# Kernel tuning notes

Hardware: AMD Instinct MI355X
Metric: run time of the kernel (lower is better)

Reference implementation:

```python
import jax, jax.numpy as jnp
import numpy as np

EMB = 1024
HEADS = 16
HEAD_DIM = EMB // HEADS
FF = 4 * EMB
EPS = 1e-5


def setup_inputs() -> dict:
    key = jax.random.key(0)
    ks = jax.random.split(key, 16)
    s = 0.02
    return {
        "x": jax.random.normal(ks[0], (2, 2048, EMB), dtype=jnp.float32),
        "ln1_g": jnp.ones((EMB,), jnp.float32),
        "ln1_b": jnp.zeros((EMB,), jnp.float32),
        "Wq": jax.random.normal(ks[1], (EMB, EMB), jnp.float32) * s,
        "bq": jnp.zeros((EMB,), jnp.float32),
        "Wk": jax.random.normal(ks[2], (EMB, EMB), jnp.float32) * s,
        "bk": jnp.zeros((EMB,), jnp.float32),
        "Wv": jax.random.normal(ks[3], (EMB, EMB), jnp.float32) * s,
        "bv": jnp.zeros((EMB,), jnp.float32),
        "Wo": jax.random.normal(ks[4], (EMB, EMB), jnp.float32) * s,
        "bo": jnp.zeros((EMB,), jnp.float32),
        "ln2_g": jnp.ones((EMB,), jnp.float32),
        "ln2_b": jnp.zeros((EMB,), jnp.float32),
        "W1": jax.random.normal(ks[5], (EMB, FF), jnp.float32) * s,
        "b1": jnp.zeros((FF,), jnp.float32),
        "W2": jax.random.normal(ks[6], (FF, EMB), jnp.float32) * s,
        "b2": jnp.zeros((EMB,), jnp.float32),
    }


def _layernorm(x, g, b):
    mu = jnp.mean(x, axis=-1, keepdims=True)
    var = jnp.var(x, axis=-1, keepdims=True)
    return (x - mu) * jax.lax.rsqrt(var + EPS) * g + b


def _attention(x, Wq, bq, Wk, bk, Wv, bv, Wo, bo):
    B, T, C = x.shape
    # [B,T,C] -> [B,H,T,Dh]
    def split(y):
        return y.reshape(B, T, HEADS, HEAD_DIM).transpose(0, 2, 1, 3)
    Q = split(x @ Wq + bq)
    K = split(x @ Wk + bk)
    V = split(x @ Wv + bv)
    att = jnp.einsum("bhqd,bhkd->bhqk", Q, K) / np.sqrt(HEAD_DIM).astype(np.float32)
    causal = jnp.tril(jnp.ones((T, T), bool))
    att = jnp.where(causal, att, -jnp.inf)
    att = jax.nn.softmax(att, axis=-1)
    out = jnp.einsum("bhqk,bhkd->bhqd", att, V)
    out = out.transpose(0, 2, 1, 3).reshape(B, T, C)
    return out @ Wo + bo


def reference(x, ln1_g, ln1_b, Wq, bq, Wk, bk, Wv, bv, Wo, bo,
              ln2_g, ln2_b, W1, b1, W2, b2):
    # dropout is identity in eval mode
    x = x + _attention(_layernorm(x, ln1_g, ln1_b), Wq, bq, Wk, bk, Wv, bv, Wo, bo)
    h = _layernorm(x, ln2_g, ln2_b)
    h = jax.nn.gelu(h @ W1 + b1, approximate=False) @ W2 + b2
    return x + h
```

## Files before the change

kernel.cpp:

```cpp
#include <hip/hip_runtime.h>
#include <hip/hip_bf16.h>

typedef __attribute__((ext_vector_type(4))) float f32x4;
typedef __attribute__((ext_vector_type(8))) short bf16x8;
typedef unsigned int u32;
typedef unsigned short u16;

#define GASP __attribute__((address_space(1)))
#define LASP __attribute__((address_space(3)))

__device__ __forceinline__ u16 f2bf(float f) {
  u32 u = __float_as_uint(f);
  return (u16)((u + 0x7fffu + ((u >> 16) & 1u)) >> 16);
}

__device__ __forceinline__ u32 cvtpk(float lo, float hi) {
  u32 r;
  asm("v_cvt_pk_bf16_f32 %0, %1, %2" : "=v"(r) : "v"(lo), "v"(hi));
  return r;
}

__device__ __forceinline__ void gl_lds16(const void* g, void* l) {
  __builtin_amdgcn_global_load_lds((const GASP u32*)g, (LASP u32*)l, 16, 0, 0);
}

struct CastArgs {
  const float* s[6];
  u16* d[6];
};

__global__ __launch_bounds__(256) void cast_w(CastArgs a) {
  int bid = blockIdx.x;
  int w, t, K, N, kshift;
  if (bid < 4096)      { w = bid >> 10; t = bid & 1023; K = 1024; N = 1024; kshift = 5; }
  else if (bid < 8192) { w = 4; t = bid - 4096; K = 1024; N = 4096; kshift = 5; }
  else                 { w = 5; t = bid - 8192; K = 4096; N = 1024; kshift = 7; }
  int tk = t & ((1 << kshift) - 1);
  int tn = t >> kshift;
  int k0 = tk << 5, n0 = tn << 5;
  const float* src = a.s[w];
  u16* dst = a.d[w];
  __shared__ u16 tile[32][36];
  int r = threadIdx.x >> 3, c0 = (threadIdx.x & 7) << 2;
  float4 v = *(const float4*)&src[(size_t)(k0 + r) * N + n0 + c0];
  tile[c0 + 0][r] = f2bf(v.x);
  tile[c0 + 1][r] = f2bf(v.y);
  tile[c0 + 2][r] = f2bf(v.z);
  tile[c0 + 3][r] = f2bf(v.w);
  __syncthreads();
  ushort4 o;
  o.x = tile[r][c0 + 0];
  o.y = tile[r][c0 + 1];
  o.z = tile[r][c0 + 2];
  o.w = tile[r][c0 + 3];
  *(ushort4*)&dst[(size_t)(n0 + r) * K + k0 + c0] = o;
}

__global__ __launch_bounds__(256) void ln_k(const float* __restrict__ x, const float* __restrict__ g,
                                            const float* __restrict__ b, u16* __restrict__ out) {
  int row = blockIdx.x;
  int tid = threadIdx.x;
  float4 v = *(const float4*)&x[(size_t)row * 1024 + tid * 4];
  float s = v.x + v.y + v.z + v.w;
  float ss = v.x * v.x + v.y * v.y + v.z * v.z + v.w * v.w;
#pragma unroll
  for (int o = 32; o >= 1; o >>= 1) {
    s += __shfl_xor(s, o, 64);
    ss += __shfl_xor(ss, o, 64);
  }
  __shared__ float red[8];
  int wv = tid >> 6;
  if ((tid & 63) == 0) { red[wv] = s; red[wv + 4] = ss; }
  __syncthreads();
  s = red[0] + red[1] + red[2] + red[3];
  ss = red[4] + red[5] + red[6] + red[7];
  float mu = s * (1.0f / 1024.0f);
  float var = ss * (1.0f / 1024.0f) - mu * mu;
  float rstd = rsqrtf(var + 1e-5f);
  float4 gv = *(const float4*)&g[tid * 4];
  float4 bv = *(const float4*)&b[tid * 4];
  ushort4 o4;
  o4.x = f2bf((v.x - mu) * rstd * gv.x + bv.x);
  o4.y = f2bf((v.y - mu) * rstd * gv.y + bv.y);
  o4.z = f2bf((v.z - mu) * rstd * gv.z + bv.z);
  o4.w = f2bf((v.w - mu) * rstd * gv.w + bv.w);
  *(ushort4*)&out[(size_t)row * 1024 + tid * 4] = o4;
}

template <int MODE>
__global__ __launch_bounds__(512, 2) void gemm_256(
    const u16* __restrict__ A, const u16* __restrict__ Bt,
    const float* __restrict__ bias0, const float* __restrict__ bias1, const float* __restrict__ bias2,
    void* outp, int rm, int rn, int xn, int M, int N, int K) {
  __shared__ __align__(16) u16 As[4][128 * 64];
  __shared__ __align__(16) u16 Bs[4][128 * 64];
  char* asB = (char*)As;
  char* bsB = (char*)Bs;
  const int tid = threadIdx.x;
  const int w = tid >> 6, lane = tid & 63;
  const int xcd = blockIdx.x & 7, idx = blockIdx.x >> 3;
  const int mt = (xcd / xn) * rm + (idx % rm);
  const int nt = (xcd % xn) * rn + (idx / rm);
  const int m0 = mt << 8, n0 = nt << 8;

  const int rA = tid >> 3;
  const int csw = ((tid & 7) ^ (rA & 7)) * 8;
  const u16* pA = A + (size_t)(m0 + rA) * K + csw;
  const u16* pB = Bt + (size_t)(n0 + rA) * K + csw;
  const int dstOff = tid * 16;

#define STG_A(kt, h, d_) do {                                            \
    const u16* s_ = pA + (size_t)((h) * 128) * K + (size_t)(kt) * 64;    \
    char* l_ = asB + ((d_) * 2 + (h)) * 16384 + dstOff;                  \
    gl_lds16(s_, l_);                                                    \
    gl_lds16(s_ + (size_t)64 * K, l_ + 8192);                            \
  } while (0)
#define STG_B(kt, h, d_) do {                                            \
    const u16* s_ = pB + (size_t)((h) * 128) * K + (size_t)(kt) * 64;    \
    char* l_ = bsB + ((d_) * 2 + (h)) * 16384 + dstOff;                  \
    gl_lds16(s_, l_);                                                    \
    gl_lds16(s_ + (size_t)64 * K, l_ + 8192);                            \
  } while (0)

  const int wr = w >> 2, wc = w & 3;
  const int g = lane >> 4, qi = lane & 15;

  int aOff[8][2], bOff[4][2];
#pragma unroll
  for (int mm = 0; mm < 8; ++mm) {
    int row = mm * 16 + qi;
#pragma unroll
    for (int ks = 0; ks < 2; ++ks)
      aOff[mm][ks] = row * 128 + (((ks * 4 + g) ^ (qi & 7)) << 4);
  }
#pragma unroll
  for (int nn = 0; nn < 4; ++nn) {
    int rowb = (wc & 1) * 64 + nn * 16 + qi;
#pragma unroll
    for (int ks = 0; ks < 2; ++ks)
      bOff[nn][ks] = rowb * 128 + (((ks * 4 + g) ^ (qi & 7)) << 4);
  }

  f32x4 acc[8][4];
#pragma unroll
  for (int i = 0; i < 8; ++i)
#pragma unroll
    for (int j = 0; j < 4; ++j) acc[i][j] = f32x4{0.f, 0.f, 0.f, 0.f};

#define MFMA16(MB, A00, A01, A10, A11) do {                                              \
    __builtin_amdgcn_s_setprio(1);                                                       \
    acc[(MB)][0] = __builtin_amdgcn_mfma_f32_16x16x32_bf16(A00, bv[0][0], acc[(MB)][0], 0, 0, 0); \
    acc[(MB)][1] = __builtin_amdgcn_mfma_f32_16x16x32_bf16(A00, bv[1][0], acc[(MB)][1], 0, 0, 0); \
    acc[(MB)][2] = __builtin_amdgcn_mfma_f32_16x16x32_bf16(A00, bv[2][0], acc[(MB)][2], 0, 0, 0); \
    acc[(MB)][3] = __builtin_amdgcn_mfma_f32_16x16x32_bf16(A00, bv[3][0], acc[(MB)][3], 0, 0, 0); \
    acc[(MB) + 1][0] = __builtin_amdgcn_mfma_f32_16x16x32_bf16(A10, bv[0][0], acc[(MB) + 1][0], 0, 0, 0); \
    acc[(MB) + 1][1] = __builtin_amdgcn_mfma_f32_16x16x32_bf16(A10, bv[1][0], acc[(MB) + 1][1], 0, 0, 0); \
    acc[(MB) + 1][2] = __builtin_amdgcn_mfma_f32_16x16x32_bf16(A10, bv[2][0], acc[(MB) + 1][2], 0, 0, 0); \
    acc[(MB) + 1][3] = __builtin_amdgcn_mfma_f32_16x16x32_bf16(A10, bv[3][0], acc[(MB) + 1][3], 0, 0, 0); \
    acc[(MB)][0] = __builtin_amdgcn_mfma_f32_16x16x32_bf16(A01, bv[0][1], acc[(MB)][0], 0, 0, 0); \
    acc[(MB)][1] = __builtin_amdgcn_mfma_f32_16x16x32_bf16(A01, bv[1][1], acc[(MB)][1], 0, 0, 0); \
    acc[(MB)][2] = __builtin_amdgcn_mfma_f32_16x16x32_bf16(A01, bv[2][1], acc[(MB)][2], 0, 0, 0); \
    acc[(MB)][3] = __builtin_amdgcn_mfma_f32_16x16x32_bf16(A01, bv[3][1], acc[(MB)][3], 0, 0, 0); \
    acc[(MB) + 1][0] = __builtin_amdgcn_mfma_f32_16x16x32_bf16(A11, bv[0][1], acc[(MB) + 1][0], 0, 0, 0); \
    acc[(MB) + 1][1] = __builtin_amdgcn_mfma_f32_16x16x32_bf16(A11, bv[1][1], acc[(MB) + 1][1], 0, 0, 0); \
    acc[(MB) + 1][2] = __builtin_amdgcn_mfma_f32_16x16x32_bf16(A11, bv[2][1], acc[(MB) + 1][2], 0, 0, 0); \
    acc[(MB) + 1][3] = __builtin_amdgcn_mfma_f32_16x16x32_bf16(A11, bv[3][1], acc[(MB) + 1][3], 0, 0, 0); \
    __builtin_amdgcn_s_setprio(0);                                                       \
  } while (0)

#define RDA(dst0, dst1, MB)                                          \
    bf16x8 dst0##0 = *(const bf16x8*)(asB + aTB + aOff[(MB)][0]);     \
    bf16x8 dst0##1 = *(const bf16x8*)(asB + aTB + aOff[(MB)][1]);     \
    bf16x8 dst1##0 = *(const bf16x8*)(asB + aTB + aOff[(MB) + 1][0]); \
    bf16x8 dst1##1 = *(const bf16x8*)(asB + aTB + aOff[(MB) + 1][1]);

  const int T = K >> 6;
  STG_A(0, 0, 0); STG_A(0, 1, 0);
  STG_B(0, 0, 0); STG_B(0, 1, 0);
  asm volatile("s_waitcnt vmcnt(0)" ::: "memory");
  __builtin_amdgcn_s_barrier();

  for (int t = 0; t < T; ++t) {
    const int d = t & 1;
    const int aTB = (d * 2 + wr) * 16384;
    const int bTB = (d * 2 + (wc >> 1)) * 16384;
    bf16x8 bv[4][2];
#pragma unroll
    for (int nn = 0; nn < 4; ++nn) {
      bv[nn][0] = *(const bf16x8*)(bsB + bTB + bOff[nn][0]);
      bv[nn][1] = *(const bf16x8*)(bsB + bTB + bOff[nn][1]);
    }
    RDA(p0a, p0b, 0);
    if (t + 1 < T) STG_A(t + 1, 0, d ^ 1);
    MFMA16(0, p0a0, p0a1, p0b0, p0b1);
    RDA(p1a, p1b, 2);
    if (t + 1 < T) STG_A(t + 1, 1, d ^ 1);
    MFMA16(2, p1a0, p1a1, p1b0, p1b1);
    RDA(p2a, p2b, 4);
    if (t + 1 < T) STG_B(t + 1, 0, d ^ 1);
    MFMA16(4, p2a0, p2a1, p2b0, p2b1);
    RDA(p3a, p3b, 6);
    if (t + 1 < T) STG_B(t + 1, 1, d ^ 1);
    MFMA16(6, p3a0, p3a1, p3b0, p3b1);
    asm volatile("" ::: "memory");
    if (t + 1 < T) { asm volatile("s_waitcnt vmcnt(0)" ::: "memory"); }
    __builtin_amdgcn_s_barrier();
  }
#undef MFMA16
#undef RDA
#undef STG_A
#undef STG_B

  const int ci = lane & 15;
#pragma unroll
  for (int mm = 0; mm < 8; ++mm) {
#pragma unroll
    for (int nn = 0; nn < 4; ++nn) {
      int colb = n0 + wc * 64 + nn * 16 + ci;
      int rowbase = m0 + wr * 128 + mm * 16 + 4 * g;
      f32x4 c = acc[mm][nn];
      if constexpr (MODE == 2) {
        int sel = colb >> 10;
        int cc = colb & 1023;
        const float* bp = sel == 0 ? bias0 : (sel == 1 ? bias1 : bias2);
        float bb = bp[cc];
        int h = cc >> 6, dd = cc & 63;
        int b_ = rowbase >> 11, tt = rowbase & 2047;
        if (sel == 2) {
          u16* op = (u16*)outp + 2ull * (4096ull * 1024ull);
          ushort4 o4;
          o4.x = f2bf(c[0] + bb);
          o4.y = f2bf(c[1] + bb);
          o4.z = f2bf(c[2] + bb);
          o4.w = f2bf(c[3] + bb);
          *(ushort4*)&op[((size_t)(b_ * 16 + h) * 64 + dd) * 2048 + tt] = o4;
        } else {
          float scale = (sel == 0) ? 0.125f : 1.0f;
          u16* op = (u16*)outp + (size_t)sel * (4096ull * 1024ull);
#pragma unroll
          for (int r = 0; r < 4; ++r)
            op[((size_t)(b_ * 16 + h) * 2048 + tt + r) * 64 + dd] = f2bf((c[r] + bb) * scale);
        }
      } else {
        float bb = bias0[colb];
#pragma unroll
        for (int r = 0; r < 4; ++r) {
          float v = c[r] + bb;
          float gl = 0.5f * v * (1.0f + erff(v * 0.70710678118654752f));
          ((u16*)outp)[(size_t)(rowbase + r) * N + colb] = f2bf(gl);
        }
      }
    }
  }
}

__global__ __launch_bounds__(512) void gemm_sk(
    const u16* __restrict__ A, const u16* __restrict__ Bt,
    const float* __restrict__ bias0, float* __restrict__ outp,
    const float* __restrict__ res, int M, int N, int K) {
  __shared__ __align__(16) union SM {
    struct { u16 As[2][4][128 * 32]; u16 Bs[2][4][128 * 32]; } t;
    float red[16][4][4][64];
  } sm;
  const int tid = threadIdx.x;
  const int w8 = tid >> 6, lane = tid & 63;
  const int gg = w8 >> 2, wl = w8 & 3;
  const int m0 = blockIdx.y << 7, n0 = blockIdx.x << 7;

  char* asB = (char*)sm.t.As[gg];
  char* bsB = (char*)sm.t.Bs[gg];
  const u16* aS[2];
  const u16* bS[2];
#pragma unroll
  for (int i = 0; i < 2; ++i) {
    int p = wl * 2048 + i * 1024 + lane * 16;
    int r = p >> 6;
    int cl = ((p >> 4) & 3) ^ ((r >> 1) & 3);
    aS[i] = A + (size_t)(m0 + r) * K + gg * 32 + cl * 8;
    bS[i] = Bt + (size_t)(n0 + r) * K + gg * 32 + cl * 8;
  }
  f32x4 acc[4][4];
#pragma unroll
  for (int i = 0; i < 4; ++i)
#pragma unroll
    for (int j = 0; j < 4; ++j) acc[i][j] = f32x4{0.f, 0.f, 0.f, 0.f};

  const int wr = wl >> 1, wc = wl & 1;
  int aOff[4], bOff[4];
#pragma unroll
  for (int mm = 0; mm < 4; ++mm) {
    int rowa = wr * 64 + mm * 16 + (lane & 15);
    aOff[mm] = rowa * 64 + (((lane >> 4) ^ ((rowa >> 1) & 3)) << 4);
    int rowb = wc * 64 + mm * 16 + (lane & 15);
    bOff[mm] = rowb * 64 + (((lane >> 4) ^ ((rowb >> 1) & 3)) << 4);
  }

  gl_lds16(aS[0], asB + wl * 2048);
  gl_lds16(aS[1], asB + wl * 2048 + 1024);
  gl_lds16(bS[0], bsB + wl * 2048);
  gl_lds16(bS[1], bsB + wl * 2048 + 1024);
  if (K > 64) {
    gl_lds16(aS[0] + 64, asB + 8192 + wl * 2048);
    gl_lds16(aS[1] + 64, asB + 8192 + wl * 2048 + 1024);
    gl_lds16(bS[0] + 64, bsB + 8192 + wl * 2048);
    gl_lds16(bS[1] + 64, bsB + 8192 + wl * 2048 + 1024);
  }
  if (K > 128) {
    gl_lds16(aS[0] + 128, asB + 16384 + wl * 2048);
    gl_lds16(aS[1] + 128, asB + 16384 + wl * 2048 + 1024);
    gl_lds16(bS[0] + 128, bsB + 16384 + wl * 2048);
    gl_lds16(bS[1] + 128, bsB + 16384 + wl * 2048 + 1024);
  }
  int buf = 0;
  for (int ks = 0; ks < K; ks += 64) {
    const int rem = ((K - ks) >> 6) - 1;
    if (rem >= 2)      { asm volatile("s_waitcnt vmcnt(8)" ::: "memory"); }
    else if (rem == 1) { asm volatile("s_waitcnt vmcnt(4)" ::: "memory"); }
    else               { asm volatile("s_waitcnt vmcnt(0)" ::: "memory"); }
    __builtin_amdgcn_s_barrier();
    asm volatile("" ::: "memory");
    if (ks + 192 < K) {
      const int nb = ((buf + 3) & 3) * 8192;
      gl_lds16(aS[0] + ks + 192, asB + nb + wl * 2048);
      gl_lds16(aS[1] + ks + 192, asB + nb + wl * 2048 + 1024);
      gl_lds16(bS[0] + ks + 192, bsB + nb + wl * 2048);
      gl_lds16(bS[1] + ks + 192, bsB + nb + wl * 2048 + 1024);
    }
    const int tb = buf * 8192;
    bf16x8 av[4], bv[4];
#pragma unroll
    for (int mm = 0; mm < 4; ++mm) av[mm] = *(const bf16x8*)(asB + tb + aOff[mm]);
#pragma unroll
    for (int nn = 0; nn < 4; ++nn) bv[nn] = *(const bf16x8*)(bsB + tb + bOff[nn]);
#pragma unroll
    for (int mm = 0; mm < 4; ++mm)
#pragma unroll
      for (int nn = 0; nn < 4; ++nn)
        acc[mm][nn] = __builtin_amdgcn_mfma_f32_16x16x32_bf16(av[mm], bv[nn], acc[mm][nn], 0, 0, 0);
    buf = (buf + 1) & 3;
  }

  __syncthreads();
  if (gg == 1) {
#pragma unroll
    for (int mm = 0; mm < 4; ++mm)
#pragma unroll
      for (int nn = 0; nn < 4; ++nn)
#pragma unroll
        for (int r = 0; r < 4; ++r) sm.red[mm * 4 + nn][r][wl][lane] = acc[mm][nn][r];
  }
  __syncthreads();
  if (gg == 0) {
    const int g = lane >> 4, ci = lane & 15;
#pragma unroll
    for (int mm = 0; mm < 4; ++mm) {
#pragma unroll
      for (int nn = 0; nn < 4; ++nn) {
        int colb = n0 + wc * 64 + nn * 16 + ci;
        int rowbase = m0 + wr * 64 + mm * 16 + 4 * g;
        float bb = bias0[colb];
#pragma unroll
        for (int r = 0; r < 4; ++r) {
          size_t idx = (size_t)(rowbase + r) * N + colb;
          outp[idx] = acc[mm][nn][r] + sm.red[mm * 4 + nn][r][wl][lane] + bb + res[idx];
        }
      }
    }
  }
}

__global__ __launch_bounds__(512) void attn_k(const u16* __restrict__ Q, const u16* __restrict__ Kg,
                                              const u16* __restrict__ Vt, u16* __restrict__ O) {
  __shared__ __align__(16) u16 Ks[2][64 * 64];
  __shared__ __align__(16) u16 Vs[2][64 * 64];
  const int bx = blockIdx.y;
  const int bh = blockIdx.x;
  const int tid = threadIdx.x, w = tid >> 6, lane = tid & 63;
  const int g = lane >> 4, qi = lane & 15;
  const u16* Qb = Q + (size_t)bh * 2048 * 64;
  const u16* Kb = Kg + (size_t)bh * 2048 * 64;
  const u16* Vtb = Vt + (size_t)bh * 64 * 2048;

  const int rS = tid >> 3, cS = tid & 7;
  const int csw = (cS ^ (rS & 7)) * 8;
  const u16* srcK = Kb + (size_t)rS * 64 + csw;
  const u16* srcV = Vtb + (size_t)rS * 2048 + csw;
  char* ksB = (char*)Ks;
  char* vsB = (char*)Vs;
  const int dstOff = tid * 16;

  int koff[4][2], voff[4][2];
#pragma unroll
  for (int t = 0; t < 4; ++t) {
    int row = 16 * t + qi;
#pragma unroll
    for (int h = 0; h < 2; ++h) koff[t][h] = row * 128 + (((4 * h + g) ^ (qi & 7)) << 4);
#pragma unroll
    for (int kt = 0; kt < 2; ++kt) voff[t][kt] = row * 128 + (((4 * kt + g) ^ (qi & 7)) << 4);
  }

  const int b_ = bh >> 4, hh = bh & 15;
  u32* Ou = (u32*)O;

  for (int job = 0; job < 2; ++job) {
    const int qt = job ? bx : 15 - bx;
    const int qmin = qt * 128 + w * 16;
    const int qrow = qmin + qi;
    const int qmaxw = qmin + 15;

    bf16x8 qf[2];
#pragma unroll
    for (int h = 0; h < 2; ++h)
      qf[h] = *(const bf16x8*)(Qb + (size_t)qrow * 64 + h * 32 + g * 8);

    f32x4 acc[4];
#pragma unroll
    for (int dt = 0; dt < 4; ++dt) acc[dt] = f32x4{0.f, 0.f, 0.f, 0.f};
    float m = -1e30f, lsum = 0.0f;

    __syncthreads();
    gl_lds16(srcK, ksB + dstOff);
    gl_lds16(srcV, vsB + dstOff);

    const int nsteps = 2 * qt + 2;
    int buf = 0;
    for (int s = 0; s < nsteps; ++s) {
      __syncthreads();
      if (s + 1 < nsteps) {
        int nb = buf ^ 1;
        gl_lds16(srcK + (size_t)(s + 1) * 4096, ksB + nb * 8192 + dstOff);
        gl_lds16(srcV + (size_t)(s + 1) * 64, vsB + nb * 8192 + dstOff);
      }
      const int kv0 = s * 64;
      if (kv0 <= qmaxw) {
        const int tb = buf * 8192;
        f32x4 st[4];
        __builtin_amdgcn_s_setprio(1);
#pragma unroll
        for (int t = 0; t < 4; ++t) {
          st[t] = f32x4{0.f, 0.f, 0.f, 0.f};
#pragma unroll
          for (int h = 0; h < 2; ++h) {
            bf16x8 kf = *(const bf16x8*)(ksB + tb + koff[t][h]);
            st[t] = __builtin_amdgcn_mfma_f32_16x16x32_bf16(kf, qf[h], st[t], 0, 0, 0);
          }
        }
        __builtin_amdgcn_s_setprio(0);
        float pvv[4][4];
        float tmax = -1e30f;
        if (kv0 + 63 > qmin) {
#pragma unroll
          for (int t = 0; t < 4; ++t)
#pragma unroll
            for (int r = 0; r < 4; ++r) {
              int key = kv0 + 16 * t + 4 * g + r;
              float sv = st[t][r];
              sv = (key <= qrow) ? sv : -1e30f;
              pvv[t][r] = sv;
              tmax = fmaxf(tmax, sv);
            }
        } else {
#pragma unroll
          for (int t = 0; t < 4; ++t)
#pragma unroll
            for (int r = 0; r < 4; ++r) {
              float sv = st[t][r];
              pvv[t][r] = sv;
              tmax = fmaxf(tmax, sv);
            }
        }
        tmax = fmaxf(tmax, __shfl_xor(tmax, 16, 64));
        tmax = fmaxf(tmax, __shfl_xor(tmax, 32, 64));
        if (!__all(tmax <= m + 8.0f)) {
          float mn = fmaxf(m, tmax);
          float corr = __expf(m - mn);
          lsum *= corr;
#pragma unroll
          for (int dt = 0; dt < 4; ++dt)
#pragma unroll
            for (int r = 0; r < 4; ++r) acc[dt][r] *= corr;
          m = mn;
        }
        float tsum = 0.f;
#pragma unroll
        for (int t = 0; t < 4; ++t)
#pragma unroll
          for (int r = 0; r < 4; ++r) {
            float e = __expf(pvv[t][r] - m);
            pvv[t][r] = e;
            tsum += e;
          }
        tsum += __shfl_xor(tsum, 16, 64);
        tsum += __shfl_xor(tsum, 32, 64);
        lsum += tsum;
        u32 pk[4][2], ex[4][2];
#pragma unroll
        for (int t = 0; t < 4; ++t)
#pragma unroll
          for (int p = 0; p < 2; ++p) {
            u32 v = cvtpk(pvv[t][2 * p], pvv[t][2 * p + 1]);
            pk[t][p] = v;
            ex[t][p] = (u32)__shfl_xor((int)v, 16, 64);
          }
        const bool ge = (g & 1) == 0;
        const bool G0 = (g >> 1) == 0;
        const bool innr = (g == 0) || (g == 3);
        u32 mm_[4][4];
#pragma unroll
        for (int t = 0; t < 4; ++t) {
          mm_[t][0] = ge ? pk[t][0] : ex[t][0];
          mm_[t][1] = ge ? pk[t][1] : ex[t][1];
          mm_[t][2] = ge ? ex[t][0] : pk[t][0];
          mm_[t][3] = ge ? ex[t][1] : pk[t][1];
        }
        union Frag { u32 u[4]; bf16x8 v; } f0, f1;
#pragma unroll
        for (int i = 0; i < 4; ++i) {
          u32 sel0 = G0 ? mm_[1][i] : mm_[0][i];
          u32 sel1 = G0 ? mm_[3][i] : mm_[2][i];
          u32 sw0 = (u32)__shfl_xor((int)sel0, 32, 64);
          u32 sw1 = (u32)__shfl_xor((int)sel1, 32, 64);
          u32 own0 = G0 ? mm_[0][i] : mm_[1][i];
          u32 own1 = G0 ? mm_[2][i] : mm_[3][i];
          f0.u[i] = innr ? own0 : sw0;
          f1.u[i] = innr ? own1 : sw1;
        }
        __builtin_amdgcn_s_setprio(1);
#pragma unroll
        for (int dt = 0; dt < 4; ++dt) {
          bf16x8 vfa = *(const bf16x8*)(vsB + tb + voff[dt][0]);
          acc[dt] = __builtin_amdgcn_mfma_f32_16x16x32_bf16(vfa, f0.v, acc[dt], 0, 0, 0);
          bf16x8 vfb = *(const bf16x8*)(vsB + tb + voff[dt][1]);
          acc[dt] = __builtin_amdgcn_mfma_f32_16x16x32_bf16(vfb, f1.v, acc[dt], 0, 0, 0);
        }
        __builtin_amdgcn_s_setprio(0);
      }
      buf ^= 1;
    }

    float rl = 1.0f / lsum;
    size_t rowq = (size_t)(b_ * 2048 + qrow);
#pragma unroll
    for (int dt = 0; dt < 4; ++dt) {
#pragma unroll
      for (int rp = 0; rp < 2; ++rp) {
        u16 lo = f2bf(acc[dt][rp * 2] * rl);
        u16 hi = f2bf(acc[dt][rp * 2 + 1] * rl);
        u32 pkd = (u32)lo | ((u32)hi << 16);
        size_t off = rowq * 1024 + hh * 64 + dt * 16 + 4 * g + rp * 2;
        Ou[off >> 1] = pkd;
      }
    }
  }
}

extern "C" void kernel_launch(void* const* d_in, const int* in_sizes, int n_in,
                              void* d_out, int out_size, void* d_ws, size_t ws_size,
                              hipStream_t stream) {
  const float* x    = (const float*)d_in[0];
  const float* ln1g = (const float*)d_in[1];
  const float* ln1b = (const float*)d_in[2];
  const float* Wq   = (const float*)d_in[3];
  const float* bq   = (const float*)d_in[4];
  const float* Wk   = (const float*)d_in[5];
  const float* bk   = (const float*)d_in[6];
  const float* Wv   = (const float*)d_in[7];
  const float* bv   = (const float*)d_in[8];
  const float* Wo   = (const float*)d_in[9];
  const float* bo   = (const float*)d_in[10];
  const float* ln2g = (const float*)d_in[11];
  const float* ln2b = (const float*)d_in[12];
  const float* W1   = (const float*)d_in[13];
  const float* b1   = (const float*)d_in[14];
  const float* W2   = (const float*)d_in[15];
  const float* b2   = (const float*)d_in[16];

  char* ws = (char*)d_ws;
  const size_t MB = 1ull << 20;
  u16* WqT = (u16*)(ws + 0 * MB);
  u16* WkT = (u16*)(ws + 2 * MB);
  u16* WvT = (u16*)(ws + 4 * MB);
  u16* WoT = (u16*)(ws + 6 * MB);
  u16* W1T = (u16*)(ws + 8 * MB);
  u16* W2T = (u16*)(ws + 16 * MB);
  u16* XN  = (u16*)(ws + 24 * MB);
  u16* Qb  = (u16*)(ws + 32 * MB);
  u16* Kb  = (u16*)(ws + 40 * MB);
  u16* Vtb = (u16*)(ws + 48 * MB);
  u16* Ob  = (u16*)(ws + 56 * MB);
  u16* Gb  = (u16*)(ws + 32 * MB);

  CastArgs ca;
  ca.s[0] = Wq; ca.s[1] = Wk; ca.s[2] = Wv; ca.s[3] = Wo; ca.s[4] = W1; ca.s[5] = W2;
  ca.d[0] = WqT; ca.d[1] = WkT; ca.d[2] = WvT; ca.d[3] = WoT; ca.d[4] = W1T; ca.d[5] = W2T;
  cast_w<<<12288, 256, 0, stream>>>(ca);

  ln_k<<<4096, 256, 0, stream>>>(x, ln1g, ln1b, XN);

  gemm_256<2><<<192, 512, 0, stream>>>(XN, WqT, bq, bk, bv, Qb, 4, 6, 2, 4096, 3072, 1024);

  attn_k<<<dim3(32, 8), 512, 0, stream>>>(Qb, Kb, Vtb, Ob);

  gemm_sk<<<dim3(8, 32), 512, 0, stream>>>(Ob, WoT, bo, (float*)d_out, x, 4096, 1024, 1024);

  ln_k<<<4096, 256, 0, stream>>>((const float*)d_out, ln2g, ln2b, XN);

  gemm_256<3><<<256, 512, 0, stream>>>(XN, W1T, b1, nullptr, nullptr, Gb, 8, 4, 4, 4096, 4096, 1024);

  gemm_sk<<<dim3(8, 32), 512, 0, stream>>>(Gb, W2T, b2, (float*)d_out, (const float*)d_out, 4096, 1024, 4096);
}
```

Measured before the change: 235.3 us.

## Restructure attention to 4 waves with two query tiles per wave sharing K/V fragments

The attention kernel now runs 256-thread blocks, where each wave owns 32 query rows (two 16-row tiles) instead of 16. K and V fragments loaded from LDS are reused across both tiles. The old two-job paired scheduling is replaced by one q-tile per block, with a 32x16 grid and launch_bounds(256,2). This halves LDS fragment reads per query and improves MFMA density, at the cost of more registers and losing the explicit causal load balancing between short and long q-tiles.

```diff
diff --git a/kernel.cpp b/kernel.cpp
--- a/kernel.cpp
+++ b/kernel.cpp
@@ -369,11 +369,11 @@
   }
 }
 
-__global__ __launch_bounds__(512) void attn_k(const u16* __restrict__ Q, const u16* __restrict__ Kg,
-                                              const u16* __restrict__ Vt, u16* __restrict__ O) {
+__global__ __launch_bounds__(256, 2) void attn_k(const u16* __restrict__ Q, const u16* __restrict__ Kg,
+                                                 const u16* __restrict__ Vt, u16* __restrict__ O) {
   __shared__ __align__(16) u16 Ks[2][64 * 64];
   __shared__ __align__(16) u16 Vs[2][64 * 64];
-  const int bx = blockIdx.y;
+  const int qt = 15 - (int)blockIdx.y;
   const int bh = blockIdx.x;
   const int tid = threadIdx.x, w = tid >> 6, lane = tid & 63;
   const int g = lane >> 4, qi = lane & 15;
@@ -381,171 +381,222 @@
   const u16* Kb = Kg + (size_t)bh * 2048 * 64;
   const u16* Vtb = Vt + (size_t)bh * 64 * 2048;
 
-  const int rS = tid >> 3, cS = tid & 7;
-  const int csw = (cS ^ (rS & 7)) * 8;
-  const u16* srcK = Kb + (size_t)rS * 64 + csw;
-  const u16* srcV = Vtb + (size_t)rS * 2048 + csw;
+  const int c1 = 256 + tid;
+  const int r0 = tid >> 3, r1 = c1 >> 3;
+  const int s0 = ((tid & 7) ^ (r0 & 7)) * 8, s1 = ((c1 & 7) ^ (r1 & 7)) * 8;
+  const u16* srcK0 = Kb + (size_t)r0 * 64 + s0;
+  const u16* srcK1 = Kb + (size_t)r1 * 64 + s1;
+  const u16* srcV0 = Vtb + (size_t)r0 * 2048 + s0;
+  const u16* srcV1 = Vtb + (size_t)r1 * 2048 + s1;
   char* ksB = (char*)Ks;
   char* vsB = (char*)Vs;
-  const int dstOff = tid * 16;
+  const int d0 = tid * 16, d1 = c1 * 16;
 
   int koff[4][2], voff[4][2];
 #pragma unroll
   for (int t = 0; t < 4; ++t) {
     int row = 16 * t + qi;
 #pragma unroll
-    for (int h = 0; h < 2; ++h) koff[t][h] = row * 128 + (((4 * h + g) ^ (qi & 7)) << 4);
-#pragma unroll
-    for (int kt = 0; kt < 2; ++kt) voff[t][kt] = row * 128 + (((4 * kt + g) ^ (qi & 7)) << 4);
+    for (int kk = 0; kk < 2; ++kk) {
+      koff[t][kk] = row * 128 + (((4 * kk + g) ^ (qi & 7)) << 4);
+      voff[t][kk] = koff[t][kk];
+    }
   }
 
   const int b_ = bh >> 4, hh = bh & 15;
   u32* Ou = (u32*)O;
 
-  for (int job = 0; job < 2; ++job) {
-    const int qt = job ? bx : 15 - bx;
-    const int qmin = qt * 128 + w * 16;
-    const int qrow = qmin + qi;
-    const int qmaxw = qmin + 15;
-
-    bf16x8 qf[2];
-#pragma unroll
-    for (int h = 0; h < 2; ++h)
-      qf[h] = *(const bf16x8*)(Qb + (size_t)qrow * 64 + h * 32 + g * 8);
-
-    f32x4 acc[4];
-#pragma unroll
-    for (int dt = 0; dt < 4; ++dt) acc[dt] = f32x4{0.f, 0.f, 0.f, 0.f};
-    float m = -1e30f, lsum = 0.0f;
-
+  const int qmin = qt * 128 + w * 32;
+  const int qr0 = qmin + qi, qr1 = qmin + 16 + qi;
+
+  bf16x8 qf[2][2];
+#pragma unroll
+  for (int h = 0; h < 2; ++h)
+#pragma unroll
+    for (int kk = 0; kk < 2; ++kk)
+      qf[h][kk] = *(const bf16x8*)(Qb + (size_t)(qmin + 16 * h + qi) * 64 + kk * 32 + g * 8);
+
+  f32x4 acc0[4], acc1[4];
+#pragma unroll
+  for (int dt = 0; dt < 4; ++dt) {
+    acc0[dt] = f32x4{0.f, 0.f, 0.f, 0.f};
+    acc1[dt] = f32x4{0.f, 0.f, 0.f, 0.f};
+  }
+  float m0 = -1e30f, l0 = 0.0f, m1 = -1e30f, l1 = 0.0f;
+
+  const bool ge = (g & 1) == 0;
+  const bool G0 = (g >> 1) == 0;
+  const bool innr = (g == 0) || (g == 3);
+  union Frag { u32 u[4]; bf16x8 v; };
+
+#define SOFTPACK(ST, ACC, MVAR, LVAR, QROW, F0, F1) do {                      \
+    float pvv[4][4];                                                          \
+    float tmax = -1e30f;                                                      \
+    if (kv0 + 63 > qmin) {                                                    \
+      _Pragma("unroll")                                                       \
+      for (int t = 0; t < 4; ++t)                                             \
+        _Pragma("unroll")                                                     \
+        for (int r = 0; r < 4; ++r) {                                         \
+          int key = kv0 + 16 * t + 4 * g + r;                                 \
+          float sv = ST[t][r];                                                \
+          sv = (key <= (QROW)) ? sv : -1e30f;                                 \
+          pvv[t][r] = sv;                                                     \
+          tmax = fmaxf(tmax, sv);                                             \
+        }                                                                     \
+    } else {                                                                  \
+      _Pragma("unroll")                                                       \
+      for (int t = 0; t < 4; ++t)                                             \
+        _Pragma("unroll")                                                     \
+        for (int r = 0; r < 4; ++r) {                                         \
+          float sv = ST[t][r];                                                \
+          pvv[t][r] = sv;                                                     \
+          tmax = fmaxf(tmax, sv);                                             \
+        }                                                                     \
+    }                                                                         \
+    tmax = fmaxf(tmax, __shfl_xor(tmax, 16, 64));                             \
+    tmax = fmaxf(tmax, __shfl_xor(tmax, 32, 64));                             \
+    if (!__all(tmax <= MVAR + 8.0f)) {                                        \
+      float mn = fmaxf(MVAR, tmax);                                           \
+      float corr = __expf(MVAR - mn);                                         \
+      LVAR *= corr;                                                           \
+      _Pragma("unroll")                                                       \
+      for (int dt = 0; dt < 4; ++dt)                                          \
+        _Pragma("unroll")                                                     \
+        for (int r = 0; r < 4; ++r) ACC[dt][r] *= corr;                       \
+      MVAR = mn;                                                              \
+    }                                                                         \
+    float tsum = 0.f;                                                         \
+    _Pragma("unroll")                                                         \
+    for (int t = 0; t < 4; ++t)                                               \
+      _Pragma("unroll")                                                       \
+      for (int r = 0; r < 4; ++r) {                                           \
+        float e = __expf(pvv[t][r] - MVAR);                                   \
+        pvv[t][r] = e;                                                        \
+        tsum += e;                                                            \
+      }                                                                       \
+    tsum += __shfl_xor(tsum, 16, 64);                                         \
+    tsum += __shfl_xor(tsum, 32, 64);                                         \
+    LVAR += tsum;                                                             \
+    u32 pk[4][2], ex[4][2];                                                   \
+    _Pragma("unroll")                                                         \
+    for (int t = 0; t < 4; ++t)                                               \
+      _Pragma("unroll")                                                       \
+      for (int p = 0; p < 2; ++p) {                                           \
+        u32 v = cvtpk(pvv[t][2 * p], pvv[t][2 * p + 1]);                      \
+        pk[t][p] = v;                                                         \
+        ex[t][p] = (u32)__shfl_xor((int)v, 16, 64);                           \
+      }                                                                       \
+    u32 mm_[4][4];                                                            \
+    _Pragma("unroll")                                                         \
+    for (int t = 0; t < 4; ++t) {                                             \
+      mm_[t][0] = ge ? pk[t][0] : ex[t][0];                                   \
+      mm_[t][1] = ge ? pk[t][1] : ex[t][1];                                   \
+      mm_[t][2] = ge ? ex[t][0] : pk[t][0];                                   \
+      mm_[t][3] = ge ? ex[t][1] : pk[t][1];                                   \
+    }                                                                         \
+    _Pragma("unroll")                                                         \
+    for (int i = 0; i < 4; ++i) {                                             \
+      u32 sel0 = G0 ? mm_[1][i] : mm_[0][i];                                  \
+      u32 sel1 = G0 ? mm_[3][i] : mm_[2][i];                                  \
+      u32 sw0 = (u32)__shfl_xor((int)sel0, 32, 64);                           \
+      u32 sw1 = (u32)__shfl_xor((int)sel1, 32, 64);                           \
+      u32 own0 = G0 ? mm_[0][i] : mm_[1][i];                                  \
+      u32 own1 = G0 ? mm_[2][i] : mm_[3][i];                                  \
+      F0.u[i] = innr ? own0 : sw0;                                            \
+      F1.u[i] = innr ? own1 : sw1;                                            \
+    }                                                                         \
+  } while (0)
+
+  gl_lds16(srcK0, ksB + d0);
+  gl_lds16(srcK1, ksB + d1);
+  gl_lds16(srcV0, vsB + d0);
+  gl_lds16(srcV1, vsB + d1);
+
+  const int nsteps = 2 * qt + 2;
+  int buf = 0;
+  for (int s = 0; s < nsteps; ++s) {
     __syncthreads();
-    gl_lds16(srcK, ksB + dstOff);
-    gl_lds16(srcV, vsB + dstOff);
-
-    const int nsteps = 2 * qt + 2;
-    int buf = 0;
-    for (int s = 0; s < nsteps; ++s) {
-      __syncthreads();
-      if (s + 1 < nsteps) {
-        int nb = buf ^ 1;
-        gl_lds16(srcK + (size_t)(s + 1) * 4096, ksB + nb * 8192 + dstOff);
-        gl_lds16(srcV + (size_t)(s + 1) * 64, vsB + nb * 8192 + dstOff);
-      }
-      const int kv0 = s * 64;
-      if (kv0 <= qmaxw) {
-        const int tb = buf * 8192;
-        f32x4 st[4];
-        __builtin_amdgcn_s_setprio(1);
-#pragma unroll
-        for (int t = 0; t < 4; ++t) {
-          st[t] = f32x4{0.f, 0.f, 0.f, 0.f};
-#pragma unroll
-          for (int h = 0; h < 2; ++h) {
-            bf16x8 kf = *(const bf16x8*)(ksB + tb + koff[t][h]);
-            st[t] = __builtin_amdgcn_mfma_f32_16x16x32_bf16(kf, qf[h], st[t], 0, 0, 0);
-          }
-        }
-        __builtin_amdgcn_s_setprio(0);
-        float pvv[4][4];
-        float tmax = -1e30f;
-        if (kv0 + 63 > qmin) {
-#pragma unroll
-          for (int t = 0; t < 4; ++t)
-#pragma unroll
-            for (int r = 0; r < 4; ++r) {
-              int key = kv0 + 16 * t + 4 * g + r;
-              float sv = st[t][r];
-              sv = (key <= qrow) ? sv : -1e30f;
-              pvv[t][r] = sv;
-              tmax = fmaxf(tmax, sv);
-            }
-        } else {
-#pragma unroll
-          for (int t = 0; t < 4; ++t)
-#pragma unroll
-            for (int r = 0; r < 4; ++r) {
-              float sv = st[t][r];
-              pvv[t][r] = sv;
-              tmax = fmaxf(tmax, sv);
-            }
-        }
-        tmax = fmaxf(tmax, __shfl_xor(tmax, 16, 64));
-        tmax = fmaxf(tmax, __shfl_xor(tmax, 32, 64));
-        if (!__all(tmax <= m + 8.0f)) {
-          float mn = fmaxf(m, tmax);
-          float corr = __expf(m - mn);
-          lsum *= corr;
-#pragma unroll
-          for (int dt = 0; dt < 4; ++dt)
-#pragma unroll
-            for (int r = 0; r < 4; ++r) acc[dt][r] *= corr;
-          m = mn;
-        }
-        float tsum = 0.f;
-#pragma unroll
-        for (int t = 0; t < 4; ++t)
-#pragma unroll
-          for (int r = 0; r < 4; ++r) {
-            float e = __expf(pvv[t][r] - m);
-            pvv[t][r] = e;
-            tsum += e;
-          }
-        tsum += __shfl_xor(tsum, 16, 64);
-        tsum += __shfl_xor(tsum, 32, 64);
-        lsum += tsum;
-        u32 pk[4][2], ex[4][2];
-#pragma unroll
-        for (int t = 0; t < 4; ++t)
-#pragma unroll
-          for (int p = 0; p < 2; ++p) {
-            u32 v = cvtpk(pvv[t][2 * p], pvv[t][2 * p + 1]);
-            pk[t][p] = v;
-            ex[t][p] = (u32)__shfl_xor((int)v, 16, 64);
-          }
-        const bool ge = (g & 1) == 0;
-        const bool G0 = (g >> 1) == 0;
-        const bool innr = (g == 0) || (g == 3);
-        u32 mm_[4][4];
-#pragma unroll
-        for (int t = 0; t < 4; ++t) {
-          mm_[t][0] = ge ? pk[t][0] : ex[t][0];
-          mm_[t][1] = ge ? pk[t][1] : ex[t][1];
-          mm_[t][2] = ge ? ex[t][0] : pk[t][0];
-          mm_[t][3] = ge ? ex[t][1] : pk[t][1];
-        }
-        union Frag { u32 u[4]; bf16x8 v; } f0, f1;
-#pragma unroll
-        for (int i = 0; i < 4; ++i) {
-          u32 sel0 = G0 ? mm_[1][i] : mm_[0][i];
-          u32 sel1 = G0 ? mm_[3][i] : mm_[2][i];
-          u32 sw0 = (u32)__shfl_xor((int)sel0, 32, 64);
-          u32 sw1 = (u32)__shfl_xor((int)sel1, 32, 64);
-          u32 own0 = G0 ? mm_[0][i] : mm_[1][i];
-          u32 own1 = G0 ? mm_[2][i] : mm_[3][i];
-          f0.u[i] = innr ? own0 : sw0;
-          f1.u[i] = innr ? own1 : sw1;
-        }
-        __builtin_amdgcn_s_setprio(1);
-#pragma unroll
-        for (int dt = 0; dt < 4; ++dt) {
-          bf16x8 vfa = *(const bf16x8*)(vsB + tb + voff[dt][0]);
-          acc[dt] = __builtin_amdgcn_mfma_f32_16x16x32_bf16(vfa, f0.v, acc[dt], 0, 0, 0);
-          bf16x8 vfb = *(const bf16x8*)(vsB + tb + voff[dt][1]);
-          acc[dt] = __builtin_amdgcn_mfma_f32_16x16x32_bf16(vfb, f1.v, acc[dt], 0, 0, 0);
-        }
-        __builtin_amdgcn_s_setprio(0);
-      }
-      buf ^= 1;
-    }
-
-    float rl = 1.0f / lsum;
-    size_t rowq = (size_t)(b_ * 2048 + qrow);
+    if (s + 1 < nsteps) {
+      int nb = buf ^ 1;
+      gl_lds16(srcK0 + (size_t)(s + 1) * 4096, ksB + nb * 8192 + d0);
+      gl_lds16(srcK1 + (size_t)(s + 1) * 4096, ksB + nb * 8192 + d1);
+      gl_lds16(srcV0 + (size_t)(s + 1) * 64, vsB + nb * 8192 + d0);
+      gl_lds16(srcV1 + (size_t)(s + 1) * 64, vsB + nb * 8192 + d1);
+    }
+    const int kv0 = s * 64;
+    if (kv0 <= qmin + 31) {
+      const int tb = buf * 8192;
+      bf16x8 kf[4][2];
+#pragma unroll
+      for (int t = 0; t < 4; ++t) {
+        kf[t][0] = *(const bf16x8*)(ksB + tb + koff[t][0]);
+        kf[t][1] = *(const bf16x8*)(ksB + tb + koff[t][1]);
+      }
+      f32x4 st0[4], st1[4];
+      __builtin_amdgcn_s_setprio(1);
+#pragma unroll
+      for (int t = 0; t < 4; ++t) {
+        st0[t] = f32x4{0.f, 0.f, 0.f, 0.f};
+        st0[t] = __builtin_amdgcn_mfma_f32_16x16x32_bf16(kf[t][0], qf[0][0], st0[t], 0, 0, 0);
+        st0[t] = __builtin_amdgcn_mfma_f32_16x16x32_bf16(kf[t][1], qf[0][1], st0[t], 0, 0, 0);
+      }
+#pragma unroll
+      for (int t = 0; t < 4; ++t) {
+        st1[t] = f32x4{0.f, 0.f, 0.f, 0.f};
+        st1[t] = __builtin_amdgcn_mfma_f32_16x16x32_bf16(kf[t][0], qf[1][0], st1[t], 0, 0, 0);
+        st1[t] = __builtin_amdgcn_mfma_f32_16x16x32_bf16(kf[t][1], qf[1][1], st1[t], 0, 0, 0);
+      }
+      __builtin_amdgcn_s_setprio(0);
+      bf16x8 vfa[4], vfb[4];
+#pragma unroll
+      for (int dt = 0; dt < 4; ++dt) {
+        vfa[dt] = *(const bf16x8*)(vsB + tb + voff[dt][0]);
+        vfb[dt] = *(const bf16x8*)(vsB + tb + voff[dt][1]);
+      }
+      Frag f00, f10, f01, f11;
+      SOFTPACK(st0, acc0, m0, l0, qr0, f00, f10);
+      SOFTPACK(st1, acc1, m1, l1, qr1, f01, f11);
+      __builtin_amdgcn_s_setprio(1);
+#pragma unroll
+      for (int dt = 0; dt < 4; ++dt) {
+        acc0[dt] = __builtin_amdgcn_mfma_f32_16x16x32_bf16(vfa[dt], f00.v, acc0[dt], 0, 0, 0);
+        acc0[dt] = __builtin_amdgcn_mfma_f32_16x16x32_bf16(vfb[dt], f10.v, acc0[dt], 0, 0, 0);
+      }
+#pragma unroll
+      for (int dt = 0; dt < 4; ++dt) {
+        acc1[dt] = __builtin_amdgcn_mfma_f32_16x16x32_bf16(vfa[dt], f01.v, acc1[dt], 0, 0, 0);
+        acc1[dt] = __builtin_amdgcn_mfma_f32_16x16x32_bf16(vfb[dt], f11.v, acc1[dt], 0, 0, 0);
+      }
+      __builtin_amdgcn_s_setprio(0);
+    }
+    buf ^= 1;
+  }
+#undef SOFTPACK
+
+  {
+    float rl = 1.0f / l0;
+    size_t rowq = (size_t)(b_ * 2048 + qr0);
 #pragma unroll
     for (int dt = 0; dt < 4; ++dt) {
 #pragma unroll
       for (int rp = 0; rp < 2; ++rp) {
-        u16 lo = f2bf(acc[dt][rp * 2] * rl);
-        u16 hi = f2bf(acc[dt][rp * 2 + 1] * rl);
+        u16 lo = f2bf(acc0[dt][rp * 2] * rl);
+        u16 hi = f2bf(acc0[dt][rp * 2 + 1] * rl);
+        u32 pkd = (u32)lo | ((u32)hi << 16);
+        size_t off = rowq * 1024 + hh * 64 + dt * 16 + 4 * g + rp * 2;
+        Ou[off >> 1] = pkd;
+      }
+    }
+  }
+  {
+    float rl = 1.0f / l1;
+    size_t rowq = (size_t)(b_ * 2048 + qr1);
+#pragma unroll
+    for (int dt = 0; dt < 4; ++dt) {
+#pragma unroll
+      for (int rp = 0; rp < 2; ++rp) {
+        u16 lo = f2bf(acc1[dt][rp * 2] * rl);
+        u16 hi = f2bf(acc1[dt][rp * 2 + 1] * rl);
         u32 pkd = (u32)lo | ((u32)hi << 16);
         size_t off = rowq * 1024 + hh * 64 + dt * 16 + 4 * g + rp * 2;
         Ou[off >> 1] = pkd;
@@ -599,7 +650,7 @@
 
   gemm_256<2><<<192, 512, 0, stream>>>(XN, WqT, bq, bk, bv, Qb, 4, 6, 2, 4096, 3072, 1024);
 
-  attn_k<<<dim3(32, 8), 512, 0, stream>>>(Qb, Kb, Vtb, Ob);
+  attn_k<<<dim3(32, 16), 256, 0, stream>>>(Qb, Kb, Vtb, Ob);
 
   gemm_sk<<<dim3(8, 32), 512, 0, stream>>>(Ob, WoT, bo, (float*)d_out, x, 4096, 1024, 1024);
 
```

Measured after the change: 246.2 us. 4.6% more time.

## Switch split-K GEMM from 4-stage to 2-stage LDS pipeline with MFMA priority

Applied to the files above, without the earlier changes.

Replaces the four-buffer, three-ahead prefetch ring in the split-K GEMM with a double buffer. The next tile's global-to-LDS loads are now issued after the current tile's LDS reads, and the code waits for all loads plus a barrier after the MFMAs. It also raises wave priority around the MFMA block. This halves LDS tile usage, which could raise occupancy, but it shortens the prefetch distance, so global latency may be less well hidden.

```diff
diff --git a/kernel.cpp b/kernel.cpp
--- a/kernel.cpp
+++ b/kernel.cpp
@@ -259,7 +259,7 @@
     const float* __restrict__ bias0, float* __restrict__ outp,
     const float* __restrict__ res, int M, int N, int K) {
   __shared__ __align__(16) union SM {
-    struct { u16 As[2][4][128 * 32]; u16 Bs[2][4][128 * 32]; } t;
+    struct { u16 As[2][2][128 * 32]; u16 Bs[2][2][128 * 32]; } t;
     float red[16][4][4][64];
   } sm;
   const int tid = threadIdx.x;
@@ -299,45 +299,35 @@
   gl_lds16(aS[1], asB + wl * 2048 + 1024);
   gl_lds16(bS[0], bsB + wl * 2048);
   gl_lds16(bS[1], bsB + wl * 2048 + 1024);
-  if (K > 64) {
-    gl_lds16(aS[0] + 64, asB + 8192 + wl * 2048);
-    gl_lds16(aS[1] + 64, asB + 8192 + wl * 2048 + 1024);
-    gl_lds16(bS[0] + 64, bsB + 8192 + wl * 2048);
-    gl_lds16(bS[1] + 64, bsB + 8192 + wl * 2048 + 1024);
-  }
-  if (K > 128) {
-    gl_lds16(aS[0] + 128, asB + 16384 + wl * 2048);
-    gl_lds16(aS[1] + 128, asB + 16384 + wl * 2048 + 1024);
-    gl_lds16(bS[0] + 128, bsB + 16384 + wl * 2048);
-    gl_lds16(bS[1] + 128, bsB + 16384 + wl * 2048 + 1024);
-  }
-  int buf = 0;
-  for (int ks = 0; ks < K; ks += 64) {
-    const int rem = ((K - ks) >> 6) - 1;
-    if (rem >= 2)      { asm volatile("s_waitcnt vmcnt(8)" ::: "memory"); }
-    else if (rem == 1) { asm volatile("s_waitcnt vmcnt(4)" ::: "memory"); }
-    else               { asm volatile("s_waitcnt vmcnt(0)" ::: "memory"); }
-    __builtin_amdgcn_s_barrier();
-    asm volatile("" ::: "memory");
-    if (ks + 192 < K) {
-      const int nb = ((buf + 3) & 3) * 8192;
-      gl_lds16(aS[0] + ks + 192, asB + nb + wl * 2048);
-      gl_lds16(aS[1] + ks + 192, asB + nb + wl * 2048 + 1024);
-      gl_lds16(bS[0] + ks + 192, bsB + nb + wl * 2048);
-      gl_lds16(bS[1] + ks + 192, bsB + nb + wl * 2048 + 1024);
+  asm volatile("s_waitcnt vmcnt(0)" ::: "memory");
+  __builtin_amdgcn_s_barrier();
+
+  const int T = K >> 6;
+  for (int t = 0; t < T; ++t) {
+    const int tb = (t & 1) * 8192;
+    const int nb = ((t & 1) ^ 1) * 8192;
+    bf16x8 av[4], bv[4];
+#pragma unroll
+    for (int mm = 0; mm < 4; ++mm) av[mm] = *(const bf16x8*)(asB + tb + aOff[mm]);
+#pragma unroll
+    for (int nn = 0; nn < 4; ++nn) bv[nn] = *(const bf16x8*)(bsB + tb + bOff[nn]);
+    if (t + 1 < T) {
+      const size_t ko = (size_t)(t + 1) * 64;
+      gl_lds16(aS[0] + ko, asB + nb + wl * 2048);
+      gl_lds16(aS[1] + ko, asB + nb + wl * 2048 + 1024);
+      gl_lds16(bS[0] + ko, bsB + nb + wl * 2048);
+      gl_lds16(bS[1] + ko, bsB + nb + wl * 2048 + 1024);
     }
-    const int tb = buf * 8192;
-    bf16x8 av[4], bv[4];
-#pragma unroll
-    for (int mm = 0; mm < 4; ++mm) av[mm] = *(const bf16x8*)(asB + tb + aOff[mm]);
-#pragma unroll
-    for (int nn = 0; nn < 4; ++nn) bv[nn] = *(const bf16x8*)(bsB + tb + bOff[nn]);
+    __builtin_amdgcn_s_setprio(1);
 #pragma unroll
     for (int mm = 0; mm < 4; ++mm)
 #pragma unroll
       for (int nn = 0; nn < 4; ++nn)
         acc[mm][nn] = __builtin_amdgcn_mfma_f32_16x16x32_bf16(av[mm], bv[nn], acc[mm][nn], 0, 0, 0);
-    buf = (buf + 1) & 3;
+    __builtin_amdgcn_s_setprio(0);
+    asm volatile("" ::: "memory");
+    if (t + 1 < T) { asm volatile("s_waitcnt vmcnt(0)" ::: "memory"); }
+    __builtin_amdgcn_s_barrier();
   }
 
   __syncthreads();
```

Result: slower. 244.7 us (+4.0%).

## Stage four KV tiles per barrier in attention kernel with double-buffered quads

Applied to the files above, without the earlier changes.

The causal attention kernel now prefetches four 64-key K/V tiles per stage into a double-buffered LDS ring and processes them between barriers. The goal is fewer __syncthreads calls and deeper prefetch of global-to-LDS loads. LDS per block grows from 32 KB to 128 KB, which likely limits each CU to one block and cuts occupancy. Tiles past the causal limit are loaded but never used.

```diff
diff --git a/kernel.cpp b/kernel.cpp
--- a/kernel.cpp
+++ b/kernel.cpp
@@ -371,8 +371,8 @@
 
 __global__ __launch_bounds__(512) void attn_k(const u16* __restrict__ Q, const u16* __restrict__ Kg,
                                               const u16* __restrict__ Vt, u16* __restrict__ O) {
-  __shared__ __align__(16) u16 Ks[2][64 * 64];
-  __shared__ __align__(16) u16 Vs[2][64 * 64];
+  __shared__ __align__(16) u16 Ks[2][4][64 * 64];
+  __shared__ __align__(16) u16 Vs[2][4][64 * 64];
   const int bx = blockIdx.y;
   const int bh = blockIdx.x;
   const int tid = threadIdx.x, w = tid >> 6, lane = tid & 63;
@@ -419,123 +419,135 @@
     float m = -1e30f, lsum = 0.0f;
 
     __syncthreads();
-    gl_lds16(srcK, ksB + dstOff);
-    gl_lds16(srcV, vsB + dstOff);
+#pragma unroll
+    for (int j = 0; j < 4; ++j) {
+      gl_lds16(srcK + (size_t)j * 4096, ksB + j * 8192 + dstOff);
+      gl_lds16(srcV + (size_t)j * 64, vsB + j * 8192 + dstOff);
+    }
 
     const int nsteps = 2 * qt + 2;
-    int buf = 0;
-    for (int s = 0; s < nsteps; ++s) {
+    const int quads = (nsteps + 3) >> 2;
+    int ph = 0;
+    for (int ss = 0; ss < quads; ++ss) {
       __syncthreads();
-      if (s + 1 < nsteps) {
-        int nb = buf ^ 1;
-        gl_lds16(srcK + (size_t)(s + 1) * 4096, ksB + nb * 8192 + dstOff);
-        gl_lds16(srcV + (size_t)(s + 1) * 64, vsB + nb * 8192 + dstOff);
+      if (ss + 1 < quads) {
+        const int nb = (ph ^ 1) * 32768;
+#pragma unroll
+        for (int j = 0; j < 4; ++j) {
+          const int sj = 4 * ss + 4 + j;
+          gl_lds16(srcK + (size_t)sj * 4096, ksB + nb + j * 8192 + dstOff);
+          gl_lds16(srcV + (size_t)sj * 64, vsB + nb + j * 8192 + dstOff);
+        }
       }
-      const int kv0 = s * 64;
-      if (kv0 <= qmaxw) {
-        const int tb = buf * 8192;
-        f32x4 st[4];
-        __builtin_amdgcn_s_setprio(1);
-#pragma unroll
-        for (int t = 0; t < 4; ++t) {
-          st[t] = f32x4{0.f, 0.f, 0.f, 0.f};
-#pragma unroll
-          for (int h = 0; h < 2; ++h) {
-            bf16x8 kf = *(const bf16x8*)(ksB + tb + koff[t][h]);
-            st[t] = __builtin_amdgcn_mfma_f32_16x16x32_bf16(kf, qf[h], st[t], 0, 0, 0);
+#pragma unroll
+      for (int j = 0; j < 4; ++j) {
+        const int s = 4 * ss + j;
+        const int kv0 = s * 64;
+        if (kv0 <= qmaxw) {
+          const int tb = ph * 32768 + j * 8192;
+          f32x4 st[4];
+          __builtin_amdgcn_s_setprio(1);
+#pragma unroll
+          for (int t = 0; t < 4; ++t) {
+            st[t] = f32x4{0.f, 0.f, 0.f, 0.f};
+#pragma unroll
+            for (int h = 0; h < 2; ++h) {
+              bf16x8 kf = *(const bf16x8*)(ksB + tb + koff[t][h]);
+              st[t] = __builtin_amdgcn_mfma_f32_16x16x32_bf16(kf, qf[h], st[t], 0, 0, 0);
+            }
           }
+          __builtin_amdgcn_s_setprio(0);
+          float pvv[4][4];
+          float tmax = -1e30f;
+          if (kv0 + 63 > qmin) {
+#pragma unroll
+            for (int t = 0; t < 4; ++t)
+#pragma unroll
+              for (int r = 0; r < 4; ++r) {
+                int key = kv0 + 16 * t + 4 * g + r;
+                float sv = st[t][r];
+                sv = (key <= qrow) ? sv : -1e30f;
+                pvv[t][r] = sv;
+                tmax = fmaxf(tmax, sv);
+              }
+          } else {
+#pragma unroll
+            for (int t = 0; t < 4; ++t)
+#pragma unroll
+              for (int r = 0; r < 4; ++r) {
+                float sv = st[t][r];
+                pvv[t][r] = sv;
+                tmax = fmaxf(tmax, sv);
+              }
+          }
+          tmax = fmaxf(tmax, __shfl_xor(tmax, 16, 64));
+          tmax = fmaxf(tmax, __shfl_xor(tmax, 32, 64));
+          if (!__all(tmax <= m + 8.0f)) {
+            float mn = fmaxf(m, tmax);
+            float corr = __expf(m - mn);
+            lsum *= corr;
+#pragma unroll
+            for (int dt = 0; dt < 4; ++dt)
+#pragma unroll
+              for (int r = 0; r < 4; ++r) acc[dt][r] *= corr;
+            m = mn;
+          }
+          float tsum = 0.f;
+#pragma unroll
+          for (int t = 0; t < 4; ++t)
+#pragma unroll
+            for (int r = 0; r < 4; ++r) {
+              float e = __expf(pvv[t][r] - m);
+              pvv[t][r] = e;
+              tsum += e;
+            }
+          tsum += __shfl_xor(tsum, 16, 64);
+          tsum += __shfl_xor(tsum, 32, 64);
+          lsum += tsum;
+          u32 pk[4][2], ex[4][2];
+#pragma unroll
+          for (int t = 0; t < 4; ++t)
+#pragma unroll
+            for (int p = 0; p < 2; ++p) {
+              u32 v = cvtpk(pvv[t][2 * p], pvv[t][2 * p + 1]);
+              pk[t][p] = v;
+              ex[t][p] = (u32)__shfl_xor((int)v, 16, 64);
+            }
+          const bool ge = (g & 1) == 0;
+          const bool G0 = (g >> 1) == 0;
+          const bool innr = (g == 0) || (g == 3);
+          u32 mm_[4][4];
+#pragma unroll
+          for (int t = 0; t < 4; ++t) {
+            mm_[t][0] = ge ? pk[t][0] : ex[t][0];
+            mm_[t][1] = ge ? pk[t][1] : ex[t][1];
+            mm_[t][2] = ge ? ex[t][0] : pk[t][0];
+            mm_[t][3] = ge ? ex[t][1] : pk[t][1];
+          }
+          union Frag { u32 u[4]; bf16x8 v; } f0, f1;
+#pragma unroll
+          for (int i = 0; i < 4; ++i) {
+            u32 sel0 = G0 ? mm_[1][i] : mm_[0][i];
+            u32 sel1 = G0 ? mm_[3][i] : mm_[2][i];
+            u32 sw0 = (u32)__shfl_xor((int)sel0, 32, 64);
+            u32 sw1 = (u32)__shfl_xor((int)sel1, 32, 64);
+            u32 own0 = G0 ? mm_[0][i] : mm_[1][i];
+            u32 own1 = G0 ? mm_[2][i] : mm_[3][i];
+            f0.u[i] = innr ? own0 : sw0;
+            f1.u[i] = innr ? own1 : sw1;
+          }
+          __builtin_amdgcn_s_setprio(1);
+#pragma unroll
+          for (int dt = 0; dt < 4; ++dt) {
+            bf16x8 vfa = *(const bf16x8*)(vsB + tb + voff[dt][0]);
+            acc[dt] = __builtin_amdgcn_mfma_f32_16x16x32_bf16(vfa, f0.v, acc[dt], 0, 0, 0);
+            bf16x8 vfb = *(const bf16x8*)(vsB + tb + voff[dt][1]);
+            acc[dt] = __builtin_amdgcn_mfma_f32_16x16x32_bf16(vfb, f1.v, acc[dt], 0, 0, 0);
+          }
+          __builtin_amdgcn_s_setprio(0);
         }
-        __builtin_amdgcn_s_setprio(0);
-        float pvv[4][4];
-        float tmax = -1e30f;
-        if (kv0 + 63 > qmin) {
-#pragma unroll
-          for (int t = 0; t < 4; ++t)
-#pragma unroll
-            for (int r = 0; r < 4; ++r) {
-              int key = kv0 + 16 * t + 4 * g + r;
-              float sv = st[t][r];
-              sv = (key <= qrow) ? sv : -1e30f;
-              pvv[t][r] = sv;
-              tmax = fmaxf(tmax, sv);
-            }
-        } else {
-#pragma unroll
-          for (int t = 0; t < 4; ++t)
-#pragma unroll
-            for (int r = 0; r < 4; ++r) {
-              float sv = st[t][r];
-              pvv[t][r] = sv;
-              tmax = fmaxf(tmax, sv);
-            }
-        }
-        tmax = fmaxf(tmax, __shfl_xor(tmax, 16, 64));
-        tmax = fmaxf(tmax, __shfl_xor(tmax, 32, 64));
-        if (!__all(tmax <= m + 8.0f)) {
-          float mn = fmaxf(m, tmax);
-          float corr = __expf(m - mn);
-          lsum *= corr;
-#pragma unroll
-          for (int dt = 0; dt < 4; ++dt)
-#pragma unroll
-            for (int r = 0; r < 4; ++r) acc[dt][r] *= corr;
-          m = mn;
-        }
-        float tsum = 0.f;
-#pragma unroll
-        for (int t = 0; t < 4; ++t)
-#pragma unroll
-          for (int r = 0; r < 4; ++r) {
-            float e = __expf(pvv[t][r] - m);
-            pvv[t][r] = e;
-            tsum += e;
-          }
-        tsum += __shfl_xor(tsum, 16, 64);
-        tsum += __shfl_xor(tsum, 32, 64);
-        lsum += tsum;
-        u32 pk[4][2], ex[4][2];
-#pragma unroll
-        for (int t = 0; t < 4; ++t)
-#pragma unroll
-          for (int p = 0; p < 2; ++p) {
-            u32 v = cvtpk(pvv[t][2 * p], pvv[t][2 * p + 1]);
-            pk[t][p] = v;
-            ex[t][p] = (u32)__shfl_xor((int)v, 16, 64);
-          }
-        const bool ge = (g & 1) == 0;
-        const bool G0 = (g >> 1) == 0;
-        const bool innr = (g == 0) || (g == 3);
-        u32 mm_[4][4];
-#pragma unroll
-        for (int t = 0; t < 4; ++t) {
-          mm_[t][0] = ge ? pk[t][0] : ex[t][0];
-          mm_[t][1] = ge ? pk[t][1] : ex[t][1];
-          mm_[t][2] = ge ? ex[t][0] : pk[t][0];
-          mm_[t][3] = ge ? ex[t][1] : pk[t][1];
-        }
-        union Frag { u32 u[4]; bf16x8 v; } f0, f1;
-#pragma unroll
-        for (int i = 0; i < 4; ++i) {
-          u32 sel0 = G0 ? mm_[1][i] : mm_[0][i];
-          u32 sel1 = G0 ? mm_[3][i] : mm_[2][i];
-          u32 sw0 = (u32)__shfl_xor((int)sel0, 32, 64);
-          u32 sw1 = (u32)__shfl_xor((int)sel1, 32, 64);
-          u32 own0 = G0 ? mm_[0][i] : mm_[1][i];
-          u32 own1 = G0 ? mm_[2][i] : mm_[3][i];
-          f0.u[i] = innr ? own0 : sw0;
-          f1.u[i] = innr ? own1 : sw1;
-        }
-        __builtin_amdgcn_s_setprio(1);
-#pragma unroll
-        for (int dt = 0; dt < 4; ++dt) {
-          bf16x8 vfa = *(const bf16x8*)(vsB + tb + voff[dt][0]);
-          acc[dt] = __builtin_amdgcn_mfma_f32_16x16x32_bf16(vfa, f0.v, acc[dt], 0, 0, 0);
-          bf16x8 vfb = *(const bf16x8*)(vsB + tb + voff[dt][1]);
-          acc[dt] = __builtin_amdgcn_mfma_f32_16x16x32_bf16(vfb, f1.v, acc[dt], 0, 0, 0);
-        }
-        __builtin_amdgcn_s_setprio(0);
       }
-      buf ^= 1;
+      ph ^= 1;
     }
 
     float rl = 1.0f / lsum;
```

Result: faster. 226.8 us (-3.6%).
